# Kernel tuning notes

Hardware: AMD Instinct MI355X
Metric: run time of the kernel (lower is better)

Reference implementation:

```python
import jax, jax.numpy as jnp
import numpy as np

B, S, D, H = 4, 2048, 2048, 16
HD = D // H  # 128
THETA = 10000.0


def setup_inputs() -> dict:
    key = jax.random.key(0)
    k1, k2, k3 = jax.random.split(key, 3)
    x = jax.random.normal(k1, (B, S, D), dtype=jnp.float32)
    wqkv = jax.random.normal(k2, (3 * D, D), dtype=jnp.float32) * (1.0 / np.sqrt(D))
    wo = jax.random.normal(k3, (D, D), dtype=jnp.float32) * (1.0 / np.sqrt(D))
    return {"x": x, "wqkv": wqkv, "wo": wo}


def _rotate_half(t):
    t1 = t[..., : t.shape[-1] // 2]
    t2 = t[..., t.shape[-1] // 2 :]
    return jnp.concatenate([-t2, t1], axis=-1)


def reference(x, wqkv, wo):
    b, s, d = x.shape
    h, hd = H, HD
    # fused QKV projection (Linear without bias: x @ W^T)
    qkv = jnp.einsum("bsd,ed->bse", x, wqkv).reshape(b, s, 3, h, hd)
    xq, xk, xv = qkv[:, :, 0], qkv[:, :, 1], qkv[:, :, 2]

    # RoPE tables (start_pos = 0)
    inv_freq = 1.0 / (THETA ** (jnp.arange(0, hd, 2, dtype=jnp.float32) / hd))
    t = jnp.arange(s, dtype=jnp.float32)
    freqs = jnp.outer(t, inv_freq)  # [s, hd/2]
    cos = jnp.concatenate([jnp.cos(freqs)] * 2, axis=-1).reshape(1, s, 1, hd)
    sin = jnp.concatenate([jnp.sin(freqs)] * 2, axis=-1).reshape(1, s, 1, hd)

    xq = xq * cos + _rotate_half(xq) * sin
    xk = xk * cos + _rotate_half(xk) * sin

    # causal SDPA (kv_cache is None, seq_len > 1)
    scale = 1.0 / np.sqrt(hd)
    scores = jnp.einsum("bqhd,bkhd->bhqk", xq, xk) * scale
    causal = jnp.tril(jnp.ones((s, s), dtype=bool))
    scores = jnp.where(causal, scores, jnp.finfo(scores.dtype).min)
    attn = jax.nn.softmax(scores, axis=-1)
    out = jnp.einsum("bhqk,bkhd->bqhd", attn, xv).reshape(b, s, d)
    return jnp.einsum("bsd,od->bso", out, wo)
```

## Files before the change

kernel.cpp:

```cpp
#include <hip/hip_runtime.h>

typedef unsigned short u16;
typedef unsigned int u32;
typedef __bf16 bf16x8 __attribute__((ext_vector_type(8)));
typedef unsigned short u16x8 __attribute__((ext_vector_type(8)));
typedef float f32x4 __attribute__((ext_vector_type(4)));

#define S_LEN 2048
#define NH 16
#define HD 128

#define AS1 __attribute__((address_space(1)))
#define AS3 __attribute__((address_space(3)))

__device__ __forceinline__ u16 f2bf(float x) {
  u32 u = __builtin_bit_cast(u32, x);
  u32 r = u + 0x7FFFu + ((u >> 16) & 1u);
  return (u16)(r >> 16);
}
__device__ __forceinline__ float bf2f(u16 b) {
  return __builtin_bit_cast(float, (u32)b << 16);
}

__global__ void cvt_xw(const float* __restrict__ x, const float* __restrict__ wq,
                       u16* __restrict__ xb, u16* __restrict__ wqb) {
  int i = blockIdx.x * 256 + threadIdx.x;
  const float* src; u16* dst;
  if (i < 4194304) { src = x; dst = xb; }
  else { i -= 4194304; src = wq; dst = wqb; }
  float4 v = ((const float4*)src)[i];
  ushort4 o;
  o.x = f2bf(v.x); o.y = f2bf(v.y); o.z = f2bf(v.z); o.w = f2bf(v.w);
  ((ushort4*)dst)[i] = o;
}

__global__ void cvt_f32_bf16(const float* __restrict__ in, u16* __restrict__ out, int n4) {
  int i = blockIdx.x * 256 + threadIdx.x;
  if (i >= n4) return;
  float4 v = ((const float4*)in)[i];
  ushort4 o;
  o.x = f2bf(v.x); o.y = f2bf(v.y); o.z = f2bf(v.z); o.w = f2bf(v.w);
  ((ushort4*)out)[i] = o;
}

__global__ void build_tab(float* __restrict__ tab) {
  int t = blockIdx.x * 256 + threadIdx.x;
  int s = t >> 6, j = t & 63;
  float inv = exp2f(-(float)j * 0.20762050593045083f);
  float ang = (float)s * inv;
  tab[t] = cosf(ang);
  tab[131072 + t] = sinf(ang);
}

__device__ __forceinline__ void storeC(u16* p, float v) { *p = f2bf(v); }
__device__ __forceinline__ void storeC(float* p, float v) { *p = v; }

template <int EPI, typename OutT>
__global__ __launch_bounds__(512, 2) void gemm_fused(const u16* __restrict__ A, const u16* __restrict__ B,
                                                     OutT* __restrict__ C, const float* __restrict__ tab,
                                                     u16* __restrict__ Qr, u16* __restrict__ Kr,
                                                     u16* __restrict__ Vt,
                                                     int M, int N, int K, int nbx) {
  __shared__ alignas(16) u16 LDS[65536];
  char* lds = (char*)LDS;
  const int tid = threadIdx.x;
  const int lane = tid & 63;
  const int w = tid >> 6;
  const int wr = w >> 2, wc = w & 3;
  const int g = lane >> 4, c = lane & 15;

  const int nwg = gridDim.x;
  const int id = blockIdx.x;
  const int sw = (id & 7) * (nwg >> 3) + (id >> 3);
  const int bx = sw % nbx, by = sw / nbx;
  const size_t rowBase = (size_t)by * 256;
  const size_t colBase = (size_t)bx * 256;

  const int half = w & 1;
  const int sub = (w >> 1) & 3;
  const size_t ldb = (size_t)K * 2;
  const int srow = lane >> 3;
  const int soff = ((lane & 7) ^ srow) << 4;
  const char* ApS = (const char*)A + (rowBase + half * 128 + srow) * ldb + soff;
  const char* BpS = (const char*)B + (colBase + half * 128 + srow) * ldb + soff;

  auto stA = [&](int u, int blk) {
    const int r0 = blk * 32 + sub * 8;
    const int dst = ((u & 1) * 2 + half) * 16384 + r0 * 128;
    __builtin_amdgcn_global_load_lds((const AS1 void*)(ApS + (size_t)r0 * ldb + (size_t)u * 128),
                                     (AS3 void*)(lds + dst), 16, 0, 0);
  };
  auto stB = [&](int u, int jj) {
    const int r0 = (sub * 4 + jj) * 8;
    const int dst = 65536 + ((u & 1) * 2 + half) * 16384 + r0 * 128;
    __builtin_amdgcn_global_load_lds((const AS1 void*)(BpS + (size_t)r0 * ldb + (size_t)u * 128),
                                     (AS3 void*)(lds + dst), 16, 0, 0);
  };

  const int dq32 = (wc & 1) * 32;
  const int swz = (c & 7) << 4;
  auto rdA = [&](int bA, int mi, int kk) -> bf16x8 {
    return *(const bf16x8*)(lds + bA + mi * 2048 + c * 128 + ((kk * 64 + g * 16) ^ swz));
  };
  auto rdB = [&](int bB, int n, int kk) -> bf16x8 {
    int row_l;
    if (EPI) row_l = dq32 + (n & 1) * 16 + ((n >= 2) ? 64 : 0) + c;
    else     row_l = (wc & 1) * 64 + n * 16 + c;
    return *(const bf16x8*)(lds + bB + row_l * 128 + ((kk * 64 + g * 16) ^ swz));
  };

  f32x4 acc[8][4];
#pragma unroll
  for (int m = 0; m < 8; ++m)
#pragma unroll
    for (int n = 0; n < 4; ++n) acc[m][n] = f32x4{0.f, 0.f, 0.f, 0.f};

  bf16x8 bf_[4][2];
  bf16x8 aP[4], aQ[4];

  auto loadA = [&](bf16x8 (&s)[4], int bA, int mi) {
    s[0] = rdA(bA, mi, 0); s[1] = rdA(bA, mi, 1);
    s[2] = rdA(bA, mi + 1, 0); s[3] = rdA(bA, mi + 1, 1);
  };
  auto loadR1 = [&](int bA, int bB) {
    loadA(aP, bA, 0);
#pragma unroll
    for (int n = 0; n < 4; ++n) { bf_[n][0] = rdB(bB, n, 0); bf_[n][1] = rdB(bB, n, 1); }
  };
  auto MFMA2 = [&](int mi, bf16x8 (&s)[4]) {
#pragma unroll
    for (int n = 0; n < 4; ++n) {
      acc[mi][n]     = __builtin_amdgcn_mfma_f32_16x16x32_bf16(s[0], bf_[n][0], acc[mi][n], 0, 0, 0);
      acc[mi][n]     = __builtin_amdgcn_mfma_f32_16x16x32_bf16(s[1], bf_[n][1], acc[mi][n], 0, 0, 0);
      acc[mi + 1][n] = __builtin_amdgcn_mfma_f32_16x16x32_bf16(s[2], bf_[n][0], acc[mi + 1][n], 0, 0, 0);
      acc[mi + 1][n] = __builtin_amdgcn_mfma_f32_16x16x32_bf16(s[3], bf_[n][1], acc[mi + 1][n], 0, 0, 0);
    }
  };

  const int NT = K >> 6;

#pragma unroll
  for (int b = 0; b < 4; ++b) stA(0, b);
#pragma unroll
  for (int j = 0; j < 4; ++j) stB(0, j);
#pragma unroll
  for (int b = 0; b < 4; ++b) stA(1, b);
#pragma unroll
  for (int j = 0; j < 4; ++j) stB(1, j);
  asm volatile("s_waitcnt vmcnt(8)" ::: "memory");
  __builtin_amdgcn_s_barrier();
  {
    const int bA0 = wr * 16384;
    const int bB0 = 65536 + (wc >> 1) * 16384;
    loadR1(bA0, bB0);
  }

#pragma unroll 1
  for (int t = 0; t < NT; ++t) {
    const int bA = (t & 1) * 32768 + wr * 16384;
    const int bB = 65536 + (t & 1) * 32768 + (wc >> 1) * 16384;
    loadA(aQ, bA, 2);
    if (t >= 1 && t + 1 < NT) stA(t + 1, 3);
    asm volatile("s_waitcnt lgkmcnt(4)" ::: "memory");
    __builtin_amdgcn_sched_barrier(0);
    __builtin_amdgcn_s_setprio(1);
    MFMA2(0, aP);
    __builtin_amdgcn_s_setprio(0);
    __builtin_amdgcn_sched_barrier(0);
    __builtin_amdgcn_s_barrier();
    loadA(aP, bA, 4);
    if (t + 2 < NT) { stA(t + 2, 0); stB(t + 2, 0); stB(t + 2, 1); }
    asm volatile("s_waitcnt lgkmcnt(4)" ::: "memory");
    __builtin_amdgcn_sched_barrier(0);
    __builtin_amdgcn_s_setprio(1);
    MFMA2(2, aQ);
    __builtin_amdgcn_s_setprio(0);
    __builtin_amdgcn_sched_barrier(0);
    __builtin_amdgcn_s_barrier();
    loadA(aQ, bA, 6);
    if (t + 2 < NT) { stA(t + 2, 1); stB(t + 2, 2); stB(t + 2, 3); }
    asm volatile("s_waitcnt lgkmcnt(4)" ::: "memory");
    __builtin_amdgcn_sched_barrier(0);
    __builtin_amdgcn_s_setprio(1);
    MFMA2(4, aP);
    __builtin_amdgcn_s_setprio(0);
    __builtin_amdgcn_sched_barrier(0);
    __builtin_amdgcn_s_barrier();
    if (t + 2 < NT) stA(t + 2, 2);
    asm volatile("s_waitcnt lgkmcnt(0)" ::: "memory");
    __builtin_amdgcn_sched_barrier(0);
    __builtin_amdgcn_s_setprio(1);
    MFMA2(6, aQ);
    __builtin_amdgcn_s_setprio(0);
    __builtin_amdgcn_sched_barrier(0);
    if (t + 2 < NT) { asm volatile("s_waitcnt vmcnt(7)" ::: "memory"); }
    else            { asm volatile("s_waitcnt vmcnt(0)" ::: "memory"); }
    __builtin_amdgcn_s_barrier();
    if (t + 1 < NT) {
      const int bA1 = ((t + 1) & 1) * 32768 + wr * 16384;
      const int bB1 = 65536 + ((t + 1) & 1) * 32768 + (wc >> 1) * 16384;
      loadR1(bA1, bB1);
    }
  }

  if (EPI == 0) {
#pragma unroll
    for (int m = 0; m < 8; ++m)
#pragma unroll
      for (int n = 0; n < 4; ++n) {
        size_t row = rowBase + wr * 128 + m * 16 + g * 4;
        size_t col = colBase + wc * 64 + n * 16 + c;
#pragma unroll
        for (int r = 0; r < 4; ++r)
          storeC(&C[(row + r) * (size_t)N + col], acc[m][n][r]);
      }
  } else {
    const int slot = (int)(colBase >> 11);
    const int h = (((int)colBase >> 7) & 15) + (wc >> 1);
    const int bidx = (int)(rowBase >> 11);
    const int sbase = ((int)rowBase & 2047) + wr * 128;

    if (slot < 2) {
      u16* dst = (slot == 0 ? Qr : Kr) + (size_t)(bidx * NH + h) * S_LEN * HD;
#pragma unroll
      for (int m = 0; m < 8; ++m)
#pragma unroll
        for (int r = 0; r < 4; ++r) {
          const int s = sbase + m * 16 + g * 4 + r;
          u16* drow = dst + (size_t)s * HD;
          const float* tc = tab + s * 64;
          const float* ts = tab + 131072 + s * 64;
#pragma unroll
          for (int n = 0; n < 2; ++n) {
            const int dlo = dq32 + n * 16 + c;
            float cs = tc[dlo], sn = ts[dlo];
            float xlo = acc[m][n][r], xhi = acc[m][n + 2][r];
            drow[dlo]      = f2bf(cs * xlo - sn * xhi);
            drow[dlo + 64] = f2bf(cs * xhi + sn * xlo);
          }
        }
    } else {
      char* lv = lds + w * 16384;
#pragma unroll
      for (int m = 0; m < 8; ++m)
#pragma unroll
        for (int n = 0; n < 4; ++n) {
          const int ld = ((n >= 2) ? 32 : 0) + (n & 1) * 16 + c;
          ushort4 pk;
          pk.x = f2bf(acc[m][n][0]); pk.y = f2bf(acc[m][n][1]);
          pk.z = f2bf(acc[m][n][2]); pk.w = f2bf(acc[m][n][3]);
          *(ushort4*)(lv + ld * 256 + ((m * 32 + g * 8) ^ ((ld & 7) << 4))) = pk;
        }
      u16* vbase = Vt + (size_t)(bidx * NH + h) * HD * S_LEN;
#pragma unroll
      for (int rr = 0; rr < 16; ++rr) {
        const int ld = rr * 4 + (lane >> 4);
        const int d = dq32 + ld + ((rr >= 8) ? 32 : 0);
        u16x8 v = *(const u16x8*)(lv + ld * 256 + (((lane & 15) * 16) ^ ((ld & 7) << 4)));
        *(u16x8*)(vbase + (size_t)d * S_LEN + sbase + (lane & 15) * 8) = v;
      }
    }
  }
}

__global__ __launch_bounds__(512, 2) void attn_fwd(const u16* __restrict__ Q, const u16* __restrict__ K,
                                                   const u16* __restrict__ Vt, u16* __restrict__ O) {
  __shared__ alignas(16) u16 Ks[2 * 64 * 128];
  __shared__ alignas(16) u16 Vs[2 * 128 * 64];
  __shared__ alignas(16) u16 Pl[8 * 32 * 64];
  const int tid = threadIdx.x;
  const int lane = tid & 63;
  const int w = tid >> 6;
  const int g = lane >> 4, c = lane & 15;
  const int bh = blockIdx.x;
  const int pair = blockIdx.y;
  const int b = bh >> 4, h = bh & 15;

  const u16* Qb = Q + (size_t)bh * S_LEN * HD;
  const u16* Kb = K + (size_t)bh * S_LEN * HD;
  const u16* Vb = Vt + (size_t)bh * HD * S_LEN;
  const float SL = 0.12751753f;
  const int swz = (c & 7) << 4;

  int ldsOff[2], srcK[2], srcV[2];
#pragma unroll
  for (int ii = 0; ii < 2; ++ii) {
    int p = (w * 2 + ii) * 1024 + lane * 16;
    ldsOff[ii] = p;
    int rk = p >> 8, ik = p & 255;
    srcK[ii] = rk * 256 + (ik ^ ((rk & 7) << 4));
    int rv = p >> 7, iv = p & 127;
    srcV[ii] = rv * (S_LEN * 2) + (iv ^ ((rv & 7) << 4));
  }
  int koff[4], voff[2];
#pragma unroll
  for (int kb = 0; kb < 4; ++kb) koff[kb] = (kb * 64 + g * 16) ^ swz;
  voff[0] = (g * 16) ^ swz;
  voff[1] = (64 + g * 16) ^ swz;
  int poff[4];
#pragma unroll
  for (int t = 0; t < 4; ++t) poff[t] = (t * 32 + g * 8) ^ swz;
  char* Pw = (char*)Pl + w * 4096;

#pragma unroll 1
  for (int ph = 0; ph < 2; ++ph) {
    const int sti = ph ? (7 - pair) : pair;
    const int q0 = sti * 256 + w * 32;

    bf16x8 qf[2][4];
#pragma unroll
    for (int qh = 0; qh < 2; ++qh)
#pragma unroll
      for (int kb = 0; kb < 4; ++kb)
        qf[qh][kb] = *(const bf16x8*)&Qb[(size_t)(q0 + qh * 16 + c) * HD + kb * 32 + g * 8];

    f32x4 acc[2][8];
#pragma unroll
    for (int qh = 0; qh < 2; ++qh)
#pragma unroll
      for (int cb = 0; cb < 8; ++cb) acc[qh][cb] = f32x4{0.f, 0.f, 0.f, 0.f};
    float m_i[2] = {-3e38f, -3e38f}, l_i[2] = {0.f, 0.f};

    const int nsteps = sti * 4 + 4;
#pragma unroll
    for (int ii = 0; ii < 2; ++ii) {
      __builtin_amdgcn_global_load_lds((const AS1 void*)((const char*)Kb + srcK[ii]),
                                       (AS3 void*)((char*)Ks + ldsOff[ii] - lane * 16), 16, 0, 0);
      __builtin_amdgcn_global_load_lds((const AS1 void*)((const char*)Vb + srcV[ii]),
                                       (AS3 void*)((char*)Vs + ldsOff[ii] - lane * 16), 16, 0, 0);
    }
    __syncthreads();
    int cur = 0;

#pragma unroll 1
    for (int st = 0; st < nsteps; ++st) {
      const int kv0 = st << 6;
      if (st + 1 < nsteps) {
        const char* kbase = (const char*)Kb + (size_t)(kv0 + 64) * 256;
        const char* vbase = (const char*)Vb + (size_t)(kv0 + 64) * 2;
        const int nb = (cur ^ 1) * 16384;
#pragma unroll
        for (int ii = 0; ii < 2; ++ii) {
          __builtin_amdgcn_global_load_lds((const AS1 void*)(kbase + srcK[ii]),
                                           (AS3 void*)((char*)Ks + nb + ldsOff[ii] - lane * 16), 16, 0, 0);
          __builtin_amdgcn_global_load_lds((const AS1 void*)(vbase + srcV[ii]),
                                           (AS3 void*)((char*)Vs + nb + ldsOff[ii] - lane * 16), 16, 0, 0);
        }
      }
      if (kv0 < q0 + 32) {
        const char* Kt = (const char*)Ks + cur * 16384;
        const char* Vtl = (const char*)Vs + cur * 16384;
        f32x4 s[2][4];
#pragma unroll
        for (int qh = 0; qh < 2; ++qh)
#pragma unroll
          for (int t = 0; t < 4; ++t) s[qh][t] = f32x4{0.f, 0.f, 0.f, 0.f};
#pragma unroll
        for (int t = 0; t < 4; ++t)
#pragma unroll
          for (int kb = 0; kb < 4; ++kb) {
            bf16x8 kf = *(const bf16x8*)(Kt + t * 4096 + c * 256 + koff[kb]);
            s[0][t] = __builtin_amdgcn_mfma_f32_16x16x32_bf16(kf, qf[0][kb], s[0][t], 0, 0, 0);
            s[1][t] = __builtin_amdgcn_mfma_f32_16x16x32_bf16(kf, qf[1][kb], s[1][t], 0, 0, 0);
          }
        if (kv0 + 63 > q0) {
#pragma unroll
          for (int qh = 0; qh < 2; ++qh) {
            const int lim = q0 + qh * 16 + c - kv0 - 4 * g;
#pragma unroll
            for (int t = 0; t < 4; ++t)
#pragma unroll
              for (int r = 0; r < 4; ++r)
                s[qh][t][r] = (16 * t + r <= lim) ? s[qh][t][r] : -3e38f;
          }
        }
        float ar[2][4];
#pragma unroll
        for (int qh = 0; qh < 2; ++qh) {
          float mx = s[qh][0][0];
#pragma unroll
          for (int t = 0; t < 4; ++t)
#pragma unroll
            for (int r = 0; r < 4; ++r) mx = fmaxf(mx, s[qh][t][r]);
          mx = fmaxf(mx, __shfl_xor(mx, 16));
          mx = fmaxf(mx, __shfl_xor(mx, 32));
          const float mn = fmaxf(m_i[qh], mx);
          const float alpha = exp2f((m_i[qh] - mn) * SL);
          float rs = 0.f;
#pragma unroll
          for (int t = 0; t < 4; ++t) {
            float p0 = exp2f((s[qh][t][0] - mn) * SL);
            float p1 = exp2f((s[qh][t][1] - mn) * SL);
            float p2 = exp2f((s[qh][t][2] - mn) * SL);
            float p3 = exp2f((s[qh][t][3] - mn) * SL);
            rs += (p0 + p1) + (p2 + p3);
            ushort4 pw;
            pw.x = f2bf(p0); pw.y = f2bf(p1); pw.z = f2bf(p2); pw.w = f2bf(p3);
            *(ushort4*)(Pw + (qh * 16 + c) * 128 + poff[t]) = pw;
          }
          rs += __shfl_xor(rs, 16);
          rs += __shfl_xor(rs, 32);
          l_i[qh] = l_i[qh] * alpha + rs;
          m_i[qh] = mn;
#pragma unroll
          for (int r = 0; r < 4; ++r) ar[qh][r] = __shfl(alpha, 4 * g + r);
        }
#pragma unroll
        for (int qh = 0; qh < 2; ++qh)
#pragma unroll
          for (int cb = 0; cb < 8; ++cb)
#pragma unroll
            for (int r = 0; r < 4; ++r) acc[qh][cb][r] *= ar[qh][r];
        bf16x8 pa[2][2];
#pragma unroll
        for (int qh = 0; qh < 2; ++qh) {
          pa[qh][0] = *(const bf16x8*)(Pw + (qh * 16 + c) * 128 + voff[0]);
          pa[qh][1] = *(const bf16x8*)(Pw + (qh * 16 + c) * 128 + voff[1]);
        }
#pragma unroll
        for (int cb = 0; cb < 8; ++cb) {
          bf16x8 vf0 = *(const bf16x8*)(Vtl + cb * 2048 + c * 128 + voff[0]);
          bf16x8 vf1 = *(const bf16x8*)(Vtl + cb * 2048 + c * 128 + voff[1]);
          acc[0][cb] = __builtin_amdgcn_mfma_f32_16x16x32_bf16(pa[0][0], vf0, acc[0][cb], 0, 0, 0);
          acc[0][cb] = __builtin_amdgcn_mfma_f32_16x16x32_bf16(pa[0][1], vf1, acc[0][cb], 0, 0, 0);
          acc[1][cb] = __builtin_amdgcn_mfma_f32_16x16x32_bf16(pa[1][0], vf0, acc[1][cb], 0, 0, 0);
          acc[1][cb] = __builtin_amdgcn_mfma_f32_16x16x32_bf16(pa[1][1], vf1, acc[1][cb], 0, 0, 0);
        }
      }
      __syncthreads();
      cur ^= 1;
    }
#pragma unroll
    for (int qh = 0; qh < 2; ++qh) {
      float linv = 1.0f / l_i[qh];
      float lr[4];
#pragma unroll
      for (int r = 0; r < 4; ++r) lr[r] = __shfl(linv, 4 * g + r);
#pragma unroll
      for (int cb = 0; cb < 8; ++cb)
#pragma unroll
        for (int r = 0; r < 4; ++r) {
          int q = q0 + qh * 16 + 4 * g + r;
          O[(((size_t)b * S_LEN + q) * NH + h) * HD + cb * 16 + c] = f2bf(acc[qh][cb][r] * lr[r]);
        }
    }
  }
}

extern "C" void kernel_launch(void* const* d_in, const int* in_sizes, int n_in,
                              void* d_out, int out_size, void* d_ws, size_t ws_size,
                              hipStream_t stream) {
  const float* x    = (const float*)d_in[0];
  const float* wqkv = (const float*)d_in[1];
  const float* wo   = (const float*)d_in[2];
  float* out = (float*)d_out;
  char* ws = (char*)d_ws;

  u16*  xb    = (u16*)(ws + 0);
  u16*  wqkvb = (u16*)(ws + 33554432);
  float* tab  = (float*)(ws + 58720256);
  u16*  wob   = (u16*)(ws + 58720256);
  u16*  Vt    = (u16*)(ws + 167772160);
  u16*  attn  = (u16*)(ws + 0);
  u16*  Qr = (u16*)d_out;
  u16*  Kr = (u16*)d_out + 16777216;

  cvt_xw<<<28672, 256, 0, stream>>>(x, wqkv, xb, wqkvb);
  build_tab<<<512, 256, 0, stream>>>(tab);

  gemm_fused<1, u16><<<768, 512, 0, stream>>>(xb, wqkvb, (u16*)nullptr, tab, Qr, Kr, Vt,
                                              8192, 6144, 2048, 24);

  cvt_f32_bf16<<<4096, 256, 0, stream>>>(wo, wob, 4194304 / 4);

  attn_fwd<<<dim3(64, 4), 512, 0, stream>>>(Qr, Kr, Vt, attn);

  gemm_fused<0, float><<<256, 512, 0, stream>>>(attn, wob, out, nullptr, nullptr, nullptr, nullptr,
                                                8192, 2048, 2048, 8);
}
```

Measured before the change: 404.5 us.

## Merge prep kernels and make QKV GEMM persistent over three tiles

Merges the x/wqkv conversion, wo conversion and RoPE table build into one prep kernel, which removes several launches. The QKV GEMM now runs 256 workgroups that each loop over three column tiles sharing the same row block. This avoids the partial second wave of 768 workgroups and gives A-panel reuse in cache. wob moves to its own workspace offset so it no longer aliases tab. The cost is a serial loop per workgroup plus an extra sync between tiles, which may reduce latency hiding across tiles.

```diff
diff --git a/kernel.cpp b/kernel.cpp
--- a/kernel.cpp
+++ b/kernel.cpp
@@ -22,40 +22,35 @@
   return __builtin_bit_cast(float, (u32)b << 16);
 }
 
-__global__ void cvt_xw(const float* __restrict__ x, const float* __restrict__ wq,
-                       u16* __restrict__ xb, u16* __restrict__ wqb) {
-  int i = blockIdx.x * 256 + threadIdx.x;
-  const float* src; u16* dst;
-  if (i < 4194304) { src = x; dst = xb; }
-  else { i -= 4194304; src = wq; dst = wqb; }
-  float4 v = ((const float4*)src)[i];
-  ushort4 o;
-  o.x = f2bf(v.x); o.y = f2bf(v.y); o.z = f2bf(v.z); o.w = f2bf(v.w);
-  ((ushort4*)dst)[i] = o;
-}
-
-__global__ void cvt_f32_bf16(const float* __restrict__ in, u16* __restrict__ out, int n4) {
-  int i = blockIdx.x * 256 + threadIdx.x;
-  if (i >= n4) return;
-  float4 v = ((const float4*)in)[i];
-  ushort4 o;
-  o.x = f2bf(v.x); o.y = f2bf(v.y); o.z = f2bf(v.z); o.w = f2bf(v.w);
-  ((ushort4*)out)[i] = o;
-}
-
-__global__ void build_tab(float* __restrict__ tab) {
-  int t = blockIdx.x * 256 + threadIdx.x;
-  int s = t >> 6, j = t & 63;
-  float inv = exp2f(-(float)j * 0.20762050593045083f);
-  float ang = (float)s * inv;
-  tab[t] = cosf(ang);
-  tab[131072 + t] = sinf(ang);
+__global__ void prep_all(const float* __restrict__ x, const float* __restrict__ wqkv,
+                         const float* __restrict__ wo, u16* __restrict__ xb,
+                         u16* __restrict__ wqb, u16* __restrict__ wob,
+                         float* __restrict__ tab) {
+  int blk = blockIdx.x;
+  if (blk < 32768) {
+    int i = blk * 256 + threadIdx.x;
+    const float* src; u16* dst;
+    if (i < 4194304) { src = x; dst = xb; }
+    else if (i < 7340032) { i -= 4194304; src = wqkv; dst = wqb; }
+    else { i -= 7340032; src = wo; dst = wob; }
+    float4 v = ((const float4*)src)[i];
+    ushort4 o;
+    o.x = f2bf(v.x); o.y = f2bf(v.y); o.z = f2bf(v.z); o.w = f2bf(v.w);
+    ((ushort4*)dst)[i] = o;
+  } else {
+    int t = (blk - 32768) * 256 + threadIdx.x;
+    int s = t >> 6, j = t & 63;
+    float inv = exp2f(-(float)j * 0.20762050593045083f);
+    float ang = (float)s * inv;
+    tab[t] = cosf(ang);
+    tab[131072 + t] = sinf(ang);
+  }
 }
 
 __device__ __forceinline__ void storeC(u16* p, float v) { *p = f2bf(v); }
 __device__ __forceinline__ void storeC(float* p, float v) { *p = v; }
 
-template <int EPI, typename OutT>
+template <int EPI, int NTILES, typename OutT>
 __global__ __launch_bounds__(512, 2) void gemm_fused(const u16* __restrict__ A, const u16* __restrict__ B,
                                                      OutT* __restrict__ C, const float* __restrict__ tab,
                                                      u16* __restrict__ Qr, u16* __restrict__ Kr,
@@ -72,192 +67,199 @@
   const int nwg = gridDim.x;
   const int id = blockIdx.x;
   const int sw = (id & 7) * (nwg >> 3) + (id >> 3);
-  const int bx = sw % nbx, by = sw / nbx;
-  const size_t rowBase = (size_t)by * 256;
-  const size_t colBase = (size_t)bx * 256;
 
   const int half = w & 1;
   const int sub = (w >> 1) & 3;
   const size_t ldb = (size_t)K * 2;
   const int srow = lane >> 3;
   const int soff = ((lane & 7) ^ srow) << 4;
-  const char* ApS = (const char*)A + (rowBase + half * 128 + srow) * ldb + soff;
-  const char* BpS = (const char*)B + (colBase + half * 128 + srow) * ldb + soff;
-
-  auto stA = [&](int u, int blk) {
-    const int r0 = blk * 32 + sub * 8;
-    const int dst = ((u & 1) * 2 + half) * 16384 + r0 * 128;
-    __builtin_amdgcn_global_load_lds((const AS1 void*)(ApS + (size_t)r0 * ldb + (size_t)u * 128),
-                                     (AS3 void*)(lds + dst), 16, 0, 0);
-  };
-  auto stB = [&](int u, int jj) {
-    const int r0 = (sub * 4 + jj) * 8;
-    const int dst = 65536 + ((u & 1) * 2 + half) * 16384 + r0 * 128;
-    __builtin_amdgcn_global_load_lds((const AS1 void*)(BpS + (size_t)r0 * ldb + (size_t)u * 128),
-                                     (AS3 void*)(lds + dst), 16, 0, 0);
-  };
-
   const int dq32 = (wc & 1) * 32;
   const int swz = (c & 7) << 4;
-  auto rdA = [&](int bA, int mi, int kk) -> bf16x8 {
-    return *(const bf16x8*)(lds + bA + mi * 2048 + c * 128 + ((kk * 64 + g * 16) ^ swz));
-  };
-  auto rdB = [&](int bB, int n, int kk) -> bf16x8 {
-    int row_l;
-    if (EPI) row_l = dq32 + (n & 1) * 16 + ((n >= 2) ? 64 : 0) + c;
-    else     row_l = (wc & 1) * 64 + n * 16 + c;
-    return *(const bf16x8*)(lds + bB + row_l * 128 + ((kk * 64 + g * 16) ^ swz));
-  };
-
-  f32x4 acc[8][4];
-#pragma unroll
-  for (int m = 0; m < 8; ++m)
-#pragma unroll
-    for (int n = 0; n < 4; ++n) acc[m][n] = f32x4{0.f, 0.f, 0.f, 0.f};
-
-  bf16x8 bf_[4][2];
-  bf16x8 aP[4], aQ[4];
-
-  auto loadA = [&](bf16x8 (&s)[4], int bA, int mi) {
-    s[0] = rdA(bA, mi, 0); s[1] = rdA(bA, mi, 1);
-    s[2] = rdA(bA, mi + 1, 0); s[3] = rdA(bA, mi + 1, 1);
-  };
-  auto loadR1 = [&](int bA, int bB) {
-    loadA(aP, bA, 0);
-#pragma unroll
-    for (int n = 0; n < 4; ++n) { bf_[n][0] = rdB(bB, n, 0); bf_[n][1] = rdB(bB, n, 1); }
-  };
-  auto MFMA2 = [&](int mi, bf16x8 (&s)[4]) {
-#pragma unroll
-    for (int n = 0; n < 4; ++n) {
-      acc[mi][n]     = __builtin_amdgcn_mfma_f32_16x16x32_bf16(s[0], bf_[n][0], acc[mi][n], 0, 0, 0);
-      acc[mi][n]     = __builtin_amdgcn_mfma_f32_16x16x32_bf16(s[1], bf_[n][1], acc[mi][n], 0, 0, 0);
-      acc[mi + 1][n] = __builtin_amdgcn_mfma_f32_16x16x32_bf16(s[2], bf_[n][0], acc[mi + 1][n], 0, 0, 0);
-      acc[mi + 1][n] = __builtin_amdgcn_mfma_f32_16x16x32_bf16(s[3], bf_[n][1], acc[mi + 1][n], 0, 0, 0);
-    }
-  };
-
   const int NT = K >> 6;
 
-#pragma unroll
-  for (int b = 0; b < 4; ++b) stA(0, b);
-#pragma unroll
-  for (int j = 0; j < 4; ++j) stB(0, j);
-#pragma unroll
-  for (int b = 0; b < 4; ++b) stA(1, b);
-#pragma unroll
-  for (int j = 0; j < 4; ++j) stB(1, j);
-  asm volatile("s_waitcnt vmcnt(8)" ::: "memory");
-  __builtin_amdgcn_s_barrier();
-  {
-    const int bA0 = wr * 16384;
-    const int bB0 = 65536 + (wc >> 1) * 16384;
-    loadR1(bA0, bB0);
-  }
-
 #pragma unroll 1
-  for (int t = 0; t < NT; ++t) {
-    const int bA = (t & 1) * 32768 + wr * 16384;
-    const int bB = 65536 + (t & 1) * 32768 + (wc >> 1) * 16384;
-    loadA(aQ, bA, 2);
-    if (t >= 1 && t + 1 < NT) stA(t + 1, 3);
-    asm volatile("s_waitcnt lgkmcnt(4)" ::: "memory");
-    __builtin_amdgcn_sched_barrier(0);
-    __builtin_amdgcn_s_setprio(1);
-    MFMA2(0, aP);
-    __builtin_amdgcn_s_setprio(0);
-    __builtin_amdgcn_sched_barrier(0);
+  for (int ti = 0; ti < NTILES; ++ti) {
+    int bx, by;
+    if (NTILES == 3) { by = sw >> 3; bx = (sw & 7) * 3 + ti; }
+    else             { bx = sw % nbx; by = sw / nbx; }
+    const size_t rowBase = (size_t)by * 256;
+    const size_t colBase = (size_t)bx * 256;
+
+    const char* ApS = (const char*)A + (rowBase + half * 128 + srow) * ldb + soff;
+    const char* BpS = (const char*)B + (colBase + half * 128 + srow) * ldb + soff;
+
+    auto stA = [&](int u, int blk) {
+      const int r0 = blk * 32 + sub * 8;
+      const int dst = ((u & 1) * 2 + half) * 16384 + r0 * 128;
+      __builtin_amdgcn_global_load_lds((const AS1 void*)(ApS + (size_t)r0 * ldb + (size_t)u * 128),
+                                       (AS3 void*)(lds + dst), 16, 0, 0);
+    };
+    auto stB = [&](int u, int jj) {
+      const int r0 = (sub * 4 + jj) * 8;
+      const int dst = 65536 + ((u & 1) * 2 + half) * 16384 + r0 * 128;
+      __builtin_amdgcn_global_load_lds((const AS1 void*)(BpS + (size_t)r0 * ldb + (size_t)u * 128),
+                                       (AS3 void*)(lds + dst), 16, 0, 0);
+    };
+    auto rdA = [&](int bA, int mi, int kk) -> bf16x8 {
+      return *(const bf16x8*)(lds + bA + mi * 2048 + c * 128 + ((kk * 64 + g * 16) ^ swz));
+    };
+    auto rdB = [&](int bB, int n, int kk) -> bf16x8 {
+      int row_l;
+      if (EPI) row_l = dq32 + (n & 1) * 16 + ((n >= 2) ? 64 : 0) + c;
+      else     row_l = (wc & 1) * 64 + n * 16 + c;
+      return *(const bf16x8*)(lds + bB + row_l * 128 + ((kk * 64 + g * 16) ^ swz));
+    };
+
+    f32x4 acc[8][4];
+#pragma unroll
+    for (int m = 0; m < 8; ++m)
+#pragma unroll
+      for (int n = 0; n < 4; ++n) acc[m][n] = f32x4{0.f, 0.f, 0.f, 0.f};
+
+    bf16x8 bf_[4][2];
+    bf16x8 aP[4], aQ[4];
+
+    auto loadA = [&](bf16x8 (&s)[4], int bA, int mi) {
+      s[0] = rdA(bA, mi, 0); s[1] = rdA(bA, mi, 1);
+      s[2] = rdA(bA, mi + 1, 0); s[3] = rdA(bA, mi + 1, 1);
+    };
+    auto loadR1 = [&](int bA, int bB) {
+      loadA(aP, bA, 0);
+#pragma unroll
+      for (int n = 0; n < 4; ++n) { bf_[n][0] = rdB(bB, n, 0); bf_[n][1] = rdB(bB, n, 1); }
+    };
+    auto MFMA2 = [&](int mi, bf16x8 (&s)[4]) {
+#pragma unroll
+      for (int n = 0; n < 4; ++n) {
+        acc[mi][n]     = __builtin_amdgcn_mfma_f32_16x16x32_bf16(s[0], bf_[n][0], acc[mi][n], 0, 0, 0);
+        acc[mi][n]     = __builtin_amdgcn_mfma_f32_16x16x32_bf16(s[1], bf_[n][1], acc[mi][n], 0, 0, 0);
+        acc[mi + 1][n] = __builtin_amdgcn_mfma_f32_16x16x32_bf16(s[2], bf_[n][0], acc[mi + 1][n], 0, 0, 0);
+        acc[mi + 1][n] = __builtin_amdgcn_mfma_f32_16x16x32_bf16(s[3], bf_[n][1], acc[mi + 1][n], 0, 0, 0);
+      }
+    };
+
+    if (NTILES > 1 && ti > 0) __syncthreads();
+
+#pragma unroll
+    for (int b = 0; b < 4; ++b) stA(0, b);
+#pragma unroll
+    for (int j = 0; j < 4; ++j) stB(0, j);
+#pragma unroll
+    for (int b = 0; b < 4; ++b) stA(1, b);
+#pragma unroll
+    for (int j = 0; j < 4; ++j) stB(1, j);
+    asm volatile("s_waitcnt vmcnt(8)" ::: "memory");
     __builtin_amdgcn_s_barrier();
-    loadA(aP, bA, 4);
-    if (t + 2 < NT) { stA(t + 2, 0); stB(t + 2, 0); stB(t + 2, 1); }
-    asm volatile("s_waitcnt lgkmcnt(4)" ::: "memory");
-    __builtin_amdgcn_sched_barrier(0);
-    __builtin_amdgcn_s_setprio(1);
-    MFMA2(2, aQ);
-    __builtin_amdgcn_s_setprio(0);
-    __builtin_amdgcn_sched_barrier(0);
-    __builtin_amdgcn_s_barrier();
-    loadA(aQ, bA, 6);
-    if (t + 2 < NT) { stA(t + 2, 1); stB(t + 2, 2); stB(t + 2, 3); }
-    asm volatile("s_waitcnt lgkmcnt(4)" ::: "memory");
-    __builtin_amdgcn_sched_barrier(0);
-    __builtin_amdgcn_s_setprio(1);
-    MFMA2(4, aP);
-    __builtin_amdgcn_s_setprio(0);
-    __builtin_amdgcn_sched_barrier(0);
-    __builtin_amdgcn_s_barrier();
-    if (t + 2 < NT) stA(t + 2, 2);
-    asm volatile("s_waitcnt lgkmcnt(0)" ::: "memory");
-    __builtin_amdgcn_sched_barrier(0);
-    __builtin_amdgcn_s_setprio(1);
-    MFMA2(6, aQ);
-    __builtin_amdgcn_s_setprio(0);
-    __builtin_amdgcn_sched_barrier(0);
-    if (t + 2 < NT) { asm volatile("s_waitcnt vmcnt(7)" ::: "memory"); }
-    else            { asm volatile("s_waitcnt vmcnt(0)" ::: "memory"); }
-    __builtin_amdgcn_s_barrier();
-    if (t + 1 < NT) {
-      const int bA1 = ((t + 1) & 1) * 32768 + wr * 16384;
-      const int bB1 = 65536 + ((t + 1) & 1) * 32768 + (wc >> 1) * 16384;
-      loadR1(bA1, bB1);
-    }
-  }
-
-  if (EPI == 0) {
-#pragma unroll
-    for (int m = 0; m < 8; ++m)
-#pragma unroll
-      for (int n = 0; n < 4; ++n) {
-        size_t row = rowBase + wr * 128 + m * 16 + g * 4;
-        size_t col = colBase + wc * 64 + n * 16 + c;
-#pragma unroll
-        for (int r = 0; r < 4; ++r)
-          storeC(&C[(row + r) * (size_t)N + col], acc[m][n][r]);
+    {
+      const int bA0 = wr * 16384;
+      const int bB0 = 65536 + (wc >> 1) * 16384;
+      loadR1(bA0, bB0);
+    }
+
+#pragma unroll 1
+    for (int t = 0; t < NT; ++t) {
+      const int bA = (t & 1) * 32768 + wr * 16384;
+      const int bB = 65536 + (t & 1) * 32768 + (wc >> 1) * 16384;
+      loadA(aQ, bA, 2);
+      if (t >= 1 && t + 1 < NT) stA(t + 1, 3);
+      asm volatile("s_waitcnt lgkmcnt(4)" ::: "memory");
+      __builtin_amdgcn_sched_barrier(0);
+      __builtin_amdgcn_s_setprio(1);
+      MFMA2(0, aP);
+      __builtin_amdgcn_s_setprio(0);
+      __builtin_amdgcn_sched_barrier(0);
+      __builtin_amdgcn_s_barrier();
+      loadA(aP, bA, 4);
+      if (t + 2 < NT) { stA(t + 2, 0); stB(t + 2, 0); stB(t + 2, 1); }
+      asm volatile("s_waitcnt lgkmcnt(4)" ::: "memory");
+      __builtin_amdgcn_sched_barrier(0);
+      __builtin_amdgcn_s_setprio(1);
+      MFMA2(2, aQ);
+      __builtin_amdgcn_s_setprio(0);
+      __builtin_amdgcn_sched_barrier(0);
+      __builtin_amdgcn_s_barrier();
+      loadA(aQ, bA, 6);
+      if (t + 2 < NT) { stA(t + 2, 1); stB(t + 2, 2); stB(t + 2, 3); }
+      asm volatile("s_waitcnt lgkmcnt(4)" ::: "memory");
+      __builtin_amdgcn_sched_barrier(0);
+      __builtin_amdgcn_s_setprio(1);
+      MFMA2(4, aP);
+      __builtin_amdgcn_s_setprio(0);
+      __builtin_amdgcn_sched_barrier(0);
+      __builtin_amdgcn_s_barrier();
+      if (t + 2 < NT) stA(t + 2, 2);
+      asm volatile("s_waitcnt lgkmcnt(0)" ::: "memory");
+      __builtin_amdgcn_sched_barrier(0);
+      __builtin_amdgcn_s_setprio(1);
+      MFMA2(6, aQ);
+      __builtin_amdgcn_s_setprio(0);
+      __builtin_amdgcn_sched_barrier(0);
+      if (t + 2 < NT) { asm volatile("s_waitcnt vmcnt(7)" ::: "memory"); }
+      else            { asm volatile("s_waitcnt vmcnt(0)" ::: "memory"); }
+      __builtin_amdgcn_s_barrier();
+      if (t + 1 < NT) {
+        const int bA1 = ((t + 1) & 1) * 32768 + wr * 16384;
+        const int bB1 = 65536 + ((t + 1) & 1) * 32768 + (wc >> 1) * 16384;
+        loadR1(bA1, bB1);
       }
-  } else {
-    const int slot = (int)(colBase >> 11);
-    const int h = (((int)colBase >> 7) & 15) + (wc >> 1);
-    const int bidx = (int)(rowBase >> 11);
-    const int sbase = ((int)rowBase & 2047) + wr * 128;
-
-    if (slot < 2) {
-      u16* dst = (slot == 0 ? Qr : Kr) + (size_t)(bidx * NH + h) * S_LEN * HD;
+    }
+
+    if (EPI == 0) {
 #pragma unroll
       for (int m = 0; m < 8; ++m)
 #pragma unroll
-        for (int r = 0; r < 4; ++r) {
-          const int s = sbase + m * 16 + g * 4 + r;
-          u16* drow = dst + (size_t)s * HD;
-          const float* tc = tab + s * 64;
-          const float* ts = tab + 131072 + s * 64;
-#pragma unroll
-          for (int n = 0; n < 2; ++n) {
-            const int dlo = dq32 + n * 16 + c;
-            float cs = tc[dlo], sn = ts[dlo];
-            float xlo = acc[m][n][r], xhi = acc[m][n + 2][r];
-            drow[dlo]      = f2bf(cs * xlo - sn * xhi);
-            drow[dlo + 64] = f2bf(cs * xhi + sn * xlo);
+        for (int n = 0; n < 4; ++n) {
+          size_t row = rowBase + wr * 128 + m * 16 + g * 4;
+          size_t col = colBase + wc * 64 + n * 16 + c;
+#pragma unroll
+          for (int r = 0; r < 4; ++r)
+            storeC(&C[(row + r) * (size_t)N + col], acc[m][n][r]);
+        }
+    } else {
+      const int slot = (int)(colBase >> 11);
+      const int h = (((int)colBase >> 7) & 15) + (wc >> 1);
+      const int bidx = (int)(rowBase >> 11);
+      const int sbase = ((int)rowBase & 2047) + wr * 128;
+
+      if (slot < 2) {
+        u16* dst = (slot == 0 ? Qr : Kr) + (size_t)(bidx * NH + h) * S_LEN * HD;
+#pragma unroll
+        for (int m = 0; m < 8; ++m)
+#pragma unroll
+          for (int r = 0; r < 4; ++r) {
+            const int s = sbase + m * 16 + g * 4 + r;
+            u16* drow = dst + (size_t)s * HD;
+            const float* tc = tab + s * 64;
+            const float* ts = tab + 131072 + s * 64;
+#pragma unroll
+            for (int n = 0; n < 2; ++n) {
+              const int dlo = dq32 + n * 16 + c;
+              float cs = tc[dlo], sn = ts[dlo];
+              float xlo = acc[m][n][r], xhi = acc[m][n + 2][r];
+              drow[dlo]      = f2bf(cs * xlo - sn * xhi);
+              drow[dlo + 64] = f2bf(cs * xhi + sn * xlo);
+            }
           }
-        }
-    } else {
-      char* lv = lds + w * 16384;
-#pragma unroll
-      for (int m = 0; m < 8; ++m)
-#pragma unroll
-        for (int n = 0; n < 4; ++n) {
-          const int ld = ((n >= 2) ? 32 : 0) + (n & 1) * 16 + c;
-          ushort4 pk;
-          pk.x = f2bf(acc[m][n][0]); pk.y = f2bf(acc[m][n][1]);
-          pk.z = f2bf(acc[m][n][2]); pk.w = f2bf(acc[m][n][3]);
-          *(ushort4*)(lv + ld * 256 + ((m * 32 + g * 8) ^ ((ld & 7) << 4))) = pk;
-        }
-      u16* vbase = Vt + (size_t)(bidx * NH + h) * HD * S_LEN;
-#pragma unroll
-      for (int rr = 0; rr < 16; ++rr) {
-        const int ld = rr * 4 + (lane >> 4);
-        const int d = dq32 + ld + ((rr >= 8) ? 32 : 0);
-        u16x8 v = *(const u16x8*)(lv + ld * 256 + (((lane & 15) * 16) ^ ((ld & 7) << 4)));
-        *(u16x8*)(vbase + (size_t)d * S_LEN + sbase + (lane & 15) * 8) = v;
+      } else {
+        char* lv = lds + w * 16384;
+#pragma unroll
+        for (int m = 0; m < 8; ++m)
+#pragma unroll
+          for (int n = 0; n < 4; ++n) {
+            const int ld = ((n >= 2) ? 32 : 0) + (n & 1) * 16 + c;
+            ushort4 pk;
+            pk.x = f2bf(acc[m][n][0]); pk.y = f2bf(acc[m][n][1]);
+            pk.z = f2bf(acc[m][n][2]); pk.w = f2bf(acc[m][n][3]);
+            *(ushort4*)(lv + ld * 256 + ((m * 32 + g * 8) ^ ((ld & 7) << 4))) = pk;
+          }
+        u16* vbase = Vt + (size_t)(bidx * NH + h) * HD * S_LEN;
+#pragma unroll
+        for (int rr = 0; rr < 16; ++rr) {
+          const int ld = rr * 4 + (lane >> 4);
+          const int d = dq32 + ld + ((rr >= 8) ? 32 : 0);
+          u16x8 v = *(const u16x8*)(lv + ld * 256 + (((lane & 15) * 16) ^ ((ld & 7) << 4)));
+          *(u16x8*)(vbase + (size_t)d * S_LEN + sbase + (lane & 15) * 8) = v;
+        }
       }
     }
   }
@@ -459,22 +461,19 @@
   u16*  xb    = (u16*)(ws + 0);
   u16*  wqkvb = (u16*)(ws + 33554432);
   float* tab  = (float*)(ws + 58720256);
-  u16*  wob   = (u16*)(ws + 58720256);
+  u16*  wob   = (u16*)(ws + 67108864);
   u16*  Vt    = (u16*)(ws + 167772160);
   u16*  attn  = (u16*)(ws + 0);
   u16*  Qr = (u16*)d_out;
   u16*  Kr = (u16*)d_out + 16777216;
 
-  cvt_xw<<<28672, 256, 0, stream>>>(x, wqkv, xb, wqkvb);
-  build_tab<<<512, 256, 0, stream>>>(tab);
-
-  gemm_fused<1, u16><<<768, 512, 0, stream>>>(xb, wqkvb, (u16*)nullptr, tab, Qr, Kr, Vt,
-                                              8192, 6144, 2048, 24);
-
-  cvt_f32_bf16<<<4096, 256, 0, stream>>>(wo, wob, 4194304 / 4);
+  prep_all<<<33280, 256, 0, stream>>>(x, wqkv, wo, xb, wqkvb, wob, tab);
+
+  gemm_fused<1, 3, u16><<<256, 512, 0, stream>>>(xb, wqkvb, (u16*)nullptr, tab, Qr, Kr, Vt,
+                                                 8192, 6144, 2048, 24);
 
   attn_fwd<<<dim3(64, 4), 512, 0, stream>>>(Qr, Kr, Vt, attn);
 
-  gemm_fused<0, float><<<256, 512, 0, stream>>>(attn, wob, out, nullptr, nullptr, nullptr, nullptr,
-                                                8192, 2048, 2048, 8);
-}
+  gemm_fused<0, 1, float><<<256, 512, 0, stream>>>(attn, wob, out, nullptr, nullptr, nullptr, nullptr,
+                                                   8192, 2048, 2048, 8);
+}
```

New measurement: 570.6 us. 41.1% more time.
